# Kernel optimization log

Measured on AMD Instinct MI355X. Metric: run time of the kernel, lower is better.

Reference implementation:

```python
import jax, jax.numpy as jnp
import numpy as np

B, S, H, R = 2, 4096, 2048, 2048
NB, CW = 16, 4
BW = R // NB


def _block_diag_linear(x, w, b):
    # x: [B,S,R]; w: [NB,BW,BW]; b: [NB,BW]
    xb = x.reshape(x.shape[0], x.shape[1], NB, BW)
    out = jnp.einsum('bsni,nij->bsnj', xb, w) + b
    return out.reshape(x.shape)


def _causal_conv1d(x, conv_w, conv_b):
    # depthwise causal temporal conv: out[t] = sum_i w[i]*x[t-CW+1+i] + b
    xp = jnp.pad(x, ((0, 0), (CW - 1, 0), (0, 0)))
    out = conv_b
    for i in range(CW):
        out = out + conv_w[i] * xp[:, i:i + x.shape[1], :]
    return out


def _rg_lru_scan(x, x_gate_pre, a_gate_pre, a_param):
    gate_x = jax.nn.sigmoid(x_gate_pre)
    gate_a = jax.nn.sigmoid(a_gate_pre)
    log_a = -8.0 * gate_a * jax.nn.softplus(a_param)  # [B,S,R]
    a = jnp.exp(log_a)
    multiplier = jnp.sqrt(-jnp.expm1(2.0 * log_a))  # sqrt(1 - a^2)
    norm_x = x * gate_x * multiplier
    # h_t = a_t * h_{t-1} + norm_x_t via parallel associative scan over time
    def combine(c1, c2):
        a1, b1 = c1
        a2, b2 = c2
        return a1 * a2, a2 * b1 + b2
    _, h = jax.lax.associative_scan(combine, (a, norm_x), axis=1)
    return h


def setup_inputs() -> dict:
    key = jax.random.key(0)
    ks = jax.random.split(key, 9)
    x = jax.random.normal(ks[0], (B, S, H), dtype=jnp.float32)
    W_xy = jax.random.normal(ks[1], (2 * R, H), dtype=jnp.float32) / np.sqrt(H)
    ig_w = jax.random.normal(ks[2], (NB, BW, BW), dtype=jnp.float32) / np.sqrt(BW)
    ig_b = jnp.zeros((NB, BW), dtype=jnp.float32)
    ag_w = jax.random.normal(ks[3], (NB, BW, BW), dtype=jnp.float32) / np.sqrt(BW)
    ag_b = jnp.zeros((NB, BW), dtype=jnp.float32)
    # forget_init: a = a_real in [0.9, 0.999]; a_param = softplus^{-1}(-log(a_real))
    unif = jax.random.uniform(ks[4], (R,), dtype=jnp.float32)
    a_real = 0.5 * jnp.log(unif * (0.999 ** 2 - 0.9 ** 2) + 0.9 ** 2 + 1e-8)
    a_param = jnp.log(jnp.expm1(-a_real))
    conv_w = jax.random.normal(ks[5], (CW, R), dtype=jnp.float32) / np.sqrt(CW * R)
    conv_b = jnp.zeros((R,), dtype=jnp.float32)
    # resid_proj is zero-init in the module; use small random so output is non-trivial
    W_resid = 0.02 * jax.random.normal(ks[6], (H, R), dtype=jnp.float32)
    return {"x": x, "W_xy": W_xy, "ig_w": ig_w, "ig_b": ig_b,
            "ag_w": ag_w, "ag_b": ag_b, "a_param": a_param,
            "conv_w": conv_w, "conv_b": conv_b, "W_resid": W_resid}


def reference(x, W_xy, ig_w, ig_b, ag_w, ag_b, a_param, conv_w, conv_b, W_resid):
    xy = jnp.einsum('bsh,rh->bsr', x, W_xy)  # [B,S,2R]
    xr, y = jnp.split(xy, 2, axis=-1)
    xc = _causal_conv1d(xr, conv_w, conv_b)
    x_gate_pre = _block_diag_linear(xc, ig_w, ig_b)
    a_gate_pre = _block_diag_linear(xc, ag_w, ag_b)
    h = _rg_lru_scan(xc, x_gate_pre, a_gate_pre, a_param)
    out = jnp.einsum('bsr,hr->bsh', jax.nn.gelu(y, approximate=False) * h, W_resid)
    return out
```

## Files before the change

kernel.cpp:

```cpp
#include <hip/hip_runtime.h>
#include <hip/hip_bf16.h>

typedef __hip_bfloat16 bf16;
typedef __attribute__((ext_vector_type(8))) short s16x8;
typedef __attribute__((ext_vector_type(4))) float f32x4;

#define B_ 2
#define S_ 4096
#define H_ 2048
#define R_ 2048
#define M_ 8192
#define NB_ 16
#define BW_ 128
#define CHUNK 64
#define NCH 64

__device__ __forceinline__ short f2b_s(float f) {
    return (short)__builtin_bit_cast(unsigned short, __float2bfloat16(f));
}
__device__ __forceinline__ float b2f_s(short s) {
    unsigned int u = ((unsigned int)(unsigned short)s) << 16;
    return __builtin_bit_cast(float, u);
}
__device__ __forceinline__ float sigm_fast(float x) { return 1.f / (1.f + __expf(-x)); }

__device__ __forceinline__ void async_g2l(const void* g, void* l) {
    __builtin_amdgcn_global_load_lds((const __attribute__((address_space(1))) void*)g,
                                     (__attribute__((address_space(3))) void*)l, 16, 0, 0);
}

__global__ __launch_bounds__(256) void cast_all(const float* __restrict__ x,
                                                const float* __restrict__ wxy,
                                                const float* __restrict__ wres,
                                                bf16* __restrict__ xbf,
                                                bf16* __restrict__ wxyb,
                                                bf16* __restrict__ wresb) {
    int idx = blockIdx.x * 256 + threadIdx.x;
    const float* in; bf16* out; int off;
    if (idx < 2097152)      { in = x;    out = xbf;   off = idx; }
    else if (idx < 3145728) { in = wxy;  out = wxyb;  off = idx - 2097152; }
    else                    { in = wres; out = wresb; off = idx - 3145728; }
    size_t i8 = (size_t)off * 8;
    float4 v0 = *(const float4*)(in + i8);
    float4 v1 = *(const float4*)(in + i8 + 4);
    s16x8 o;
    o[0] = f2b_s(v0.x); o[1] = f2b_s(v0.y); o[2] = f2b_s(v0.z); o[3] = f2b_s(v0.w);
    o[4] = f2b_s(v1.x); o[5] = f2b_s(v1.y); o[6] = f2b_s(v1.z); o[7] = f2b_s(v1.w);
    *(s16x8*)(out + i8) = o;
}

__global__ __launch_bounds__(256) void wcast_T(const float* __restrict__ igw,
                                               const float* __restrict__ agw,
                                               bf16* __restrict__ wT) {
    __shared__ float tile[128 * 129];
    int blk = blockIdx.x;
    int p = blk >> 4, n = blk & 15;
    const float* w = (p ? agw : igw) + (size_t)n * 16384;
    int tid = threadIdx.x;
#pragma unroll
    for (int it = 0; it < 64; ++it) {
        int u = it * 256 + tid;
        tile[(u >> 7) * 129 + (u & 127)] = w[u];
    }
    __syncthreads();
    bf16* o = wT + (size_t)blk * 16384;
#pragma unroll
    for (int it = 0; it < 64; ++it) {
        int u = it * 256 + tid;
        o[u] = __float2bfloat16(tile[(u & 127) * 129 + (u >> 7)]);
    }
}

__global__ __launch_bounds__(256) void sp8_kernel(const float* __restrict__ apar,
                                                  float* __restrict__ sp8) {
    int r = blockIdx.x * 256 + threadIdx.x;
    float ap = apar[r];
    sp8[r] = 8.f * (ap > 20.f ? ap : log1pf(expf(ap)));
}

__device__ __forceinline__ void store_c(float* p, float v) { *p = v; }
__device__ __forceinline__ void store_c(bf16* p, float v) { *p = __float2bfloat16(v); }

template <typename OutT>
__global__ __launch_bounds__(256, 4) void gemm_bt(const bf16* __restrict__ A,
                                                  const bf16* __restrict__ Bm,
                                                  OutT* __restrict__ C,
                                                  int K, int lda, int ldb, int ldc) {
    __shared__ __align__(16) short As[128 * 64];
    __shared__ __align__(16) short Bs[128 * 64];
    const int tid = threadIdx.x;
    const int lane = tid & 63, wave = tid >> 6;
    const int waveM = wave >> 1, waveN = wave & 1;
    const int mBase = blockIdx.y * 128, nBase = blockIdx.x * 128;
    const int fm = lane & 15, q = lane >> 4;

    f32x4 acc[4][4];
#pragma unroll
    for (int i = 0; i < 4; ++i)
#pragma unroll
        for (int j = 0; j < 4; ++j) acc[i][j] = (f32x4){0.f, 0.f, 0.f, 0.f};

    for (int k0 = 0; k0 < K; k0 += 64) {
        __syncthreads();
#pragma unroll
        for (int it = 0; it < 4; ++it) {
            int off = it * 4096 + tid * 16;
            int r = off >> 7;
            int g = ((off & 127) >> 4) ^ (r & 7);
            async_g2l(A + (size_t)(mBase + r) * lda + k0 + g * 8, (char*)As + off);
            async_g2l(Bm + (size_t)(nBase + r) * ldb + k0 + g * 8, (char*)Bs + off);
        }
        __syncthreads();
#pragma unroll
        for (int s = 0; s < 2; ++s) {
            s16x8 af[4], bfr[4];
#pragma unroll
            for (int i = 0; i < 4; ++i) {
                int row = waveM * 64 + i * 16 + fm;
                af[i] = *(const s16x8*)((char*)As + row * 128 + ((((s << 2) + q) ^ (row & 7)) << 4));
                int col = waveN * 64 + i * 16 + fm;
                bfr[i] = *(const s16x8*)((char*)Bs + col * 128 + ((((s << 2) + q) ^ (col & 7)) << 4));
            }
#pragma unroll
            for (int i = 0; i < 4; ++i)
#pragma unroll
                for (int j = 0; j < 4; ++j)
                    acc[i][j] = __builtin_amdgcn_mfma_f32_16x16x32_bf16(af[i], bfr[j], acc[i][j], 0, 0, 0);
        }
    }
#pragma unroll
    for (int i = 0; i < 4; ++i) {
        int rowg = mBase + waveM * 64 + i * 16 + q * 4;
#pragma unroll
        for (int j = 0; j < 4; ++j) {
            int colg = nBase + waveN * 64 + j * 16 + fm;
#pragma unroll
            for (int rr = 0; rr < 4; ++rr)
                store_c(C + (size_t)(rowg + rr) * ldc + colg, acc[i][j][rr]);
        }
    }
}

__global__ __launch_bounds__(256) void gate_kernel(const bf16* __restrict__ xy,
                                                   const float* __restrict__ cw,
                                                   const float* __restrict__ cb,
                                                   const bf16* __restrict__ wT,
                                                   const float* __restrict__ igb,
                                                   const float* __restrict__ agb,
                                                   const float* __restrict__ sp8,
                                                   bf16* __restrict__ hloc_out,
                                                   bf16* __restrict__ cum_out,
                                                   float* __restrict__ Ach,
                                                   float* __restrict__ Hla) {
    __shared__ __align__(16) short As[64 * 128];
    __shared__ __align__(16) char  Wmem[128 * 256];
    short* Xs   = (short*)Wmem;
    short* Ws   = (short*)Wmem;
    float* a_sh = (float*)Wmem;
    const int n = blockIdx.x;
    const int mBase = blockIdx.y * 64;
    const int tid = threadIdx.x;
    const int lane = tid & 63, wave = tid >> 6;
    const int fm = lane & 15, q = lane >> 4;
    const int t0 = mBase & (S_ - 1);

#pragma unroll
    for (int it = 0; it < 5; ++it) {
        int u = it * 256 + tid;
        if (u < 67 * 16) {
            int rr = u >> 4, gg = u & 15;
            s16x8 v = (s16x8){0, 0, 0, 0, 0, 0, 0, 0};
            if (t0 != 0 || rr >= 3) {
                int m = mBase + rr - 3;
                v = *(const s16x8*)(xy + (size_t)m * 4096 + n * BW_ + gg * 8);
            }
            *(s16x8*)((char*)Xs + u * 16) = v;
        }
    }
    __syncthreads();

    {
        int col = tid & 127, rh = tid >> 7;
        int rbase = n * BW_ + col;
        float w0c = cw[rbase], w1c = cw[R_ + rbase], w2c = cw[2 * R_ + rbase],
              w3c = cw[3 * R_ + rbase];
        float bc = cb[rbase];
        int r0 = rh * 32;
        float xm3 = b2f_s(Xs[(r0 + 0) * 128 + col]);
        float xm2 = b2f_s(Xs[(r0 + 1) * 128 + col]);
        float xm1 = b2f_s(Xs[(r0 + 2) * 128 + col]);
#pragma unroll
        for (int rw = 0; rw < 32; ++rw) {
            int row = r0 + rw;
            float x0 = b2f_s(Xs[(row + 3) * 128 + col]);
            float v = bc + w0c * xm3 + w1c * xm2 + w2c * xm1 + w3c * x0;
            xm3 = xm2; xm2 = xm1; xm1 = x0;
            *(short*)((char*)As + row * 256 + ((((col >> 3)) ^ (row & 15)) << 4) +
                      (col & 7) * 2) = f2b_s(v);
        }
    }
    __syncthreads();

    const bf16* w0 = wT + (size_t)n * 16384;
#pragma unroll
    for (int it = 0; it < 8; ++it) {
        int off = it * 4096 + tid * 16;
        int j = off >> 8;
        int g = ((off & 255) >> 4) ^ (j & 15);
        async_g2l(w0 + j * 128 + g * 8, (char*)Ws + off);
    }
    __syncthreads();

    f32x4 accI[8], accA[8];
#pragma unroll
    for (int jj = 0; jj < 8; ++jj) {
        accI[jj] = (f32x4){0.f, 0.f, 0.f, 0.f};
        accA[jj] = (f32x4){0.f, 0.f, 0.f, 0.f};
    }

    const int row = wave * 16 + fm;
#pragma unroll
    for (int s = 0; s < 4; ++s) {
        s16x8 af = *(const s16x8*)((char*)As + row * 256 + ((((s << 2) + q) ^ (row & 15)) << 4));
#pragma unroll
        for (int jj = 0; jj < 8; ++jj) {
            int wrow = jj * 16 + fm;
            s16x8 bw = *(const s16x8*)((char*)Ws + wrow * 256 + ((((s << 2) + q) ^ (wrow & 15)) << 4));
            accI[jj] = __builtin_amdgcn_mfma_f32_16x16x32_bf16(af, bw, accI[jj], 0, 0, 0);
        }
    }
    __syncthreads();
    const bf16* w1 = wT + (size_t)(NB_ + n) * 16384;
#pragma unroll
    for (int it = 0; it < 8; ++it) {
        int off = it * 4096 + tid * 16;
        int j = off >> 8;
        int g = ((off & 255) >> 4) ^ (j & 15);
        async_g2l(w1 + j * 128 + g * 8, (char*)Ws + off);
    }
    __syncthreads();
#pragma unroll
    for (int s = 0; s < 4; ++s) {
        s16x8 af = *(const s16x8*)((char*)As + row * 256 + ((((s << 2) + q) ^ (row & 15)) << 4));
#pragma unroll
        for (int jj = 0; jj < 8; ++jj) {
            int wrow = jj * 16 + fm;
            s16x8 bw = *(const s16x8*)((char*)Ws + wrow * 256 + ((((s << 2) + q) ^ (wrow & 15)) << 4));
            accA[jj] = __builtin_amdgcn_mfma_f32_16x16x32_bf16(af, bw, accA[jj], 0, 0, 0);
        }
    }
    __syncthreads();

#pragma unroll
    for (int jj = 0; jj < 8; ++jj) {
        int col = jj * 16 + fm;
        int r = n * BW_ + col;
        float bi = igb[r], ba = agb[r];
        float s8 = sp8[r];
#pragma unroll
        for (int rr = 0; rr < 4; ++rr) {
            int rowl = wave * 16 + q * 4 + rr;
            short* slot = (short*)((char*)As + rowl * 256 +
                          ((((col >> 3)) ^ (rowl & 15)) << 4) + (col & 7) * 2);
            float xcv = b2f_s(*slot);
            float xg = accI[jj][rr] + bi;
            float ag = accA[jj][rr] + ba;
            float la = -s8 * sigm_fast(ag);
            float av = __expf(la);
            float t2 = 2.f * la;
            float nem = (t2 > -0.125f)
                ? -t2 * (1.f + t2 * (0.5f + t2 * (0.16666667f + t2 * 0.04166667f)))
                : 1.f - av * av;
            float nxv = xcv * sigm_fast(xg) * sqrtf(nem);
            short nxs = f2b_s(nxv);
            a_sh[rowl * 128 + col] = av;
            *slot = nxs;
        }
    }
    __syncthreads();

    if (tid < 128) {
        int col = tid;
        float h = 0.f, cum = 1.f;
        size_t o = (size_t)mBase * R_ + n * BW_ + col;
#pragma unroll 4
        for (int t = 0; t < CHUNK; ++t) {
            float a = a_sh[t * 128 + col];
            float nxv = b2f_s(*(const short*)((char*)As + t * 256 +
                              ((((col >> 3)) ^ (t & 15)) << 4) + (col & 7) * 2));
            h = fmaf(a, h, nxv);
            cum *= a;
            hloc_out[o] = __float2bfloat16(h);
            cum_out[o]  = __float2bfloat16(cum);
            o += R_;
        }
        int b = mBase >> 12, c = (mBase & (S_ - 1)) >> 6;
        int so = ((b * NCH + c) << 11) + n * BW_ + col;
        Ach[so] = cum;
        Hla[so] = h;
    }
}

__global__ __launch_bounds__(256) void scan_carry(const float* __restrict__ Ach,
                                                  const float* __restrict__ Hla,
                                                  float* __restrict__ carry) {
    int idx = blockIdx.x * 256 + threadIdx.x;
    int r = idx & (R_ - 1), b = idx >> 11;
    float cy = 0.f;
#pragma unroll 4
    for (int c = 0; c < NCH; ++c) {
        int o = (b * NCH + c) * R_ + r;
        carry[o] = cy;
        cy = fmaf(Ach[o], cy, Hla[o]);
    }
}

__global__ __launch_bounds__(256) void scan_passB(const bf16* __restrict__ hloc,
                                                  const bf16* __restrict__ cum,
                                                  const float* __restrict__ carry,
                                                  const bf16* __restrict__ xy,
                                                  bf16* __restrict__ g_out) {
    int idx = blockIdx.x * 256 + threadIdx.x;
    int m = idx >> 8;
    int r = (idx & 255) << 3;
    int b = m >> 12, c = (m & 4095) >> 6;
    int so = ((b * NCH + c) << 11) + r;
    size_t o = (size_t)m * R_ + r;
    s16x8 hv = *(const s16x8*)(hloc + o);
    s16x8 cv = *(const s16x8*)(cum + o);
    float4 cy0 = *(const float4*)(carry + so);
    float4 cy1 = *(const float4*)(carry + so + 4);
    s16x8 yv = *(const s16x8*)(xy + (size_t)m * 4096 + 2048 + r);
    float cya0 = cy0.x, cya1 = cy0.y, cya2 = cy0.z, cya3 = cy0.w;
    float cya4 = cy1.x, cya5 = cy1.y, cya6 = cy1.z, cya7 = cy1.w;
    s16x8 g;
#pragma unroll 8
    for (int i = 0; i < 8; ++i) {
        float cy = (i == 0) ? cya0 : (i == 1) ? cya1 : (i == 2) ? cya2 : (i == 3) ? cya3
                 : (i == 4) ? cya4 : (i == 5) ? cya5 : (i == 6) ? cya6 : cya7;
        float h = fmaf(b2f_s(cv[i]), cy, b2f_s(hv[i]));
        float y = b2f_s(yv[i]);
        float gg = 0.5f * y * (1.f + erff(y * 0.70710678f));
        g[i] = f2b_s(gg * h);
    }
    *(s16x8*)(g_out + o) = g;
}

extern "C" void kernel_launch(void* const* d_in, const int* in_sizes, int n_in,
                              void* d_out, int out_size, void* d_ws, size_t ws_size,
                              hipStream_t stream) {
    const float* x    = (const float*)d_in[0];
    const float* Wxy  = (const float*)d_in[1];
    const float* igw  = (const float*)d_in[2];
    const float* igb  = (const float*)d_in[3];
    const float* agw  = (const float*)d_in[4];
    const float* agb  = (const float*)d_in[5];
    const float* apar = (const float*)d_in[6];
    const float* cw   = (const float*)d_in[7];
    const float* cb   = (const float*)d_in[8];
    const float* Wres = (const float*)d_in[9];
    float* out = (float*)d_out;

    char* ws = (char*)d_ws;
    const size_t MiB = (size_t)1 << 20;
    bf16*  xbf   = (bf16*)(ws);
    bf16*  hloc  = (bf16*)(ws);
    bf16*  wxyb  = (bf16*)(ws + 32 * MiB);
    bf16*  wT    = (bf16*)(ws + 32 * MiB);
    float* sp8   = (float*)(ws + 33 * MiB + 65536);
    bf16*  xy    = (bf16*)(ws + 48 * MiB);
    bf16*  wresb = (bf16*)(ws + 112 * MiB);
    bf16*  g     = (bf16*)(ws + 120 * MiB);
    bf16*  cum   = (bf16*)(ws + 152 * MiB);
    float* Ach   = (float*)(ws + 184 * MiB);
    float* Hla   = (float*)(ws + 185 * MiB);
    float* cyb   = (float*)(ws + 186 * MiB);

    cast_all<<<14336, 256, 0, stream>>>(x, Wxy, Wres, xbf, wxyb, wresb);

    gemm_bt<bf16><<<dim3(32, 64), 256, 0, stream>>>(xbf, wxyb, xy, 2048, 2048, 2048, 4096);

    wcast_T<<<32, 256, 0, stream>>>(igw, agw, wT);
    sp8_kernel<<<8, 256, 0, stream>>>(apar, sp8);

    gate_kernel<<<dim3(NB_, 128), 256, 0, stream>>>(xy, cw, cb, wT, igb, agb, sp8,
                                                    hloc, cum, Ach, Hla);

    scan_carry<<<16, 256, 0, stream>>>(Ach, Hla, cyb);
    scan_passB<<<8192, 256, 0, stream>>>(hloc, cum, cyb, xy, g);

    gemm_bt<float><<<dim3(16, 64), 256, 0, stream>>>(g, wresb, out, 2048, 2048, 2048, 2048);
}
```

Before: 463.5 us.

## Replace 128x128 GEMM with 256x256 double-buffered, phase-pipelined 8-wave kernel

```diff
diff --git a/kernel.cpp b/kernel.cpp
--- a/kernel.cpp
+++ b/kernel.cpp
@@ -81,59 +81,116 @@
 __device__ __forceinline__ void store_c(float* p, float v) { *p = v; }
 __device__ __forceinline__ void store_c(bf16* p, float v) { *p = __float2bfloat16(v); }
 
+#define MFMA16(Q)                                                                     \
+    _Pragma("unroll") for (int j = 0; j < 4; ++j) {                                   \
+        acc[2*(Q)][j]   = __builtin_amdgcn_mfma_f32_16x16x32_bf16(af[0][0], bfr[j][0], acc[2*(Q)][j], 0, 0, 0);   \
+        acc[2*(Q)][j]   = __builtin_amdgcn_mfma_f32_16x16x32_bf16(af[0][1], bfr[j][1], acc[2*(Q)][j], 0, 0, 0);   \
+        acc[2*(Q)+1][j] = __builtin_amdgcn_mfma_f32_16x16x32_bf16(af[1][0], bfr[j][0], acc[2*(Q)+1][j], 0, 0, 0); \
+        acc[2*(Q)+1][j] = __builtin_amdgcn_mfma_f32_16x16x32_bf16(af[1][1], bfr[j][1], acc[2*(Q)+1][j], 0, 0, 0); \
+    }
+
+#define PHASE(BASEP, Q, LOADB, STMTS, VMSTMT)                                         \
+    rdA2(BASEP, Q, af);                                                               \
+    if (LOADB) rdB8(BASEP, bfr);                                                      \
+    STMTS;                                                                            \
+    if (LOADB) asm volatile("s_waitcnt lgkmcnt(8)" ::: "memory");                     \
+    __builtin_amdgcn_s_barrier();                                                     \
+    asm volatile("s_waitcnt lgkmcnt(0)" ::: "memory");                                \
+    __builtin_amdgcn_sched_barrier(0);                                                \
+    __builtin_amdgcn_s_setprio(1);                                                    \
+    MFMA16(Q);                                                                        \
+    __builtin_amdgcn_s_setprio(0);                                                    \
+    VMSTMT;                                                                           \
+    __builtin_amdgcn_s_barrier();                                                     \
+    __builtin_amdgcn_sched_barrier(0);
+
 template <typename OutT>
-__global__ __launch_bounds__(256, 4) void gemm_bt(const bf16* __restrict__ A,
+__global__ __launch_bounds__(512, 2) void gemm256(const bf16* __restrict__ A,
                                                   const bf16* __restrict__ Bm,
                                                   OutT* __restrict__ C,
                                                   int K, int lda, int ldb, int ldc) {
-    __shared__ __align__(16) short As[128 * 64];
-    __shared__ __align__(16) short Bs[128 * 64];
+    extern __shared__ __align__(16) char lds[];
     const int tid = threadIdx.x;
     const int lane = tid & 63, wave = tid >> 6;
-    const int waveM = wave >> 1, waveN = wave & 1;
-    const int mBase = blockIdx.y * 128, nBase = blockIdx.x * 128;
+    const int wm = wave >> 2, wn = wave & 3;
     const int fm = lane & 15, q = lane >> 4;
-
-    f32x4 acc[4][4];
-#pragma unroll
-    for (int i = 0; i < 4; ++i)
+    const int mBase = blockIdx.y * 256, nBase = blockIdx.x * 256;
+    const int NT = K >> 6, LT = (NT >> 1) - 1;
+
+    auto stage_half = [&](int tile, int hh) {
+        if (tile >= NT) return;
+        const bf16* src = (hh < 2) ? Bm : A;
+        const int ld = (hh < 2) ? ldb : lda;
+        const int rowBase = ((hh < 2) ? nBase : mBase) + ((hh & 1) << 7);
+        char* dst = lds + ((tile & 1) << 16) + ((hh < 2) ? 32768 : 0) + ((hh & 1) << 14);
+#pragma unroll
+        for (int rnd = 0; rnd < 2; ++rnd) {
+            int off = rnd * 8192 + tid * 16;
+            int r = off >> 7;
+            int g = ((off >> 4) & 7) ^ (r & 7);
+            async_g2l(src + (size_t)(rowBase + r) * ld + tile * 64 + g * 8, dst + off);
+        }
+    };
+    auto rdA2 = [&](const char* base, int qp, s16x8 (&dst)[2][2]) {
+#pragma unroll
+        for (int i2 = 0; i2 < 2; ++i2) {
+            int r7 = (qp * 2 + i2) * 16 + fm;
+            const char* p = base + (wm << 14) + r7 * 128;
+#pragma unroll
+            for (int kk = 0; kk < 2; ++kk)
+                dst[i2][kk] = *(const s16x8*)(p + ((((kk << 2) + q) ^ (r7 & 7)) << 4));
+        }
+    };
+    auto rdB8 = [&](const char* base, s16x8 (&dst)[4][2]) {
+#pragma unroll
+        for (int j = 0; j < 4; ++j) {
+            int col = wn * 64 + j * 16 + fm;
+            const char* p = base + 32768 + ((col >> 7) << 14) + (col & 127) * 128;
+#pragma unroll
+            for (int kk = 0; kk < 2; ++kk)
+                dst[j][kk] = *(const s16x8*)(p + ((((kk << 2) + q) ^ (col & 7)) << 4));
+        }
+    };
+
+    s16x8 af[2][2], bfr[4][2];
+    f32x4 acc[8][4];
+#pragma unroll
+    for (int i = 0; i < 8; ++i)
 #pragma unroll
         for (int j = 0; j < 4; ++j) acc[i][j] = (f32x4){0.f, 0.f, 0.f, 0.f};
 
-    for (int k0 = 0; k0 < K; k0 += 64) {
-        __syncthreads();
-#pragma unroll
-        for (int it = 0; it < 4; ++it) {
-            int off = it * 4096 + tid * 16;
-            int r = off >> 7;
-            int g = ((off & 127) >> 4) ^ (r & 7);
-            async_g2l(A + (size_t)(mBase + r) * lda + k0 + g * 8, (char*)As + off);
-            async_g2l(Bm + (size_t)(nBase + r) * ldb + k0 + g * 8, (char*)Bs + off);
-        }
-        __syncthreads();
-#pragma unroll
-        for (int s = 0; s < 2; ++s) {
-            s16x8 af[4], bfr[4];
-#pragma unroll
-            for (int i = 0; i < 4; ++i) {
-                int row = waveM * 64 + i * 16 + fm;
-                af[i] = *(const s16x8*)((char*)As + row * 128 + ((((s << 2) + q) ^ (row & 7)) << 4));
-                int col = waveN * 64 + i * 16 + fm;
-                bfr[i] = *(const s16x8*)((char*)Bs + col * 128 + ((((s << 2) + q) ^ (col & 7)) << 4));
-            }
-#pragma unroll
-            for (int i = 0; i < 4; ++i)
-#pragma unroll
-                for (int j = 0; j < 4; ++j)
-                    acc[i][j] = __builtin_amdgcn_mfma_f32_16x16x32_bf16(af[i], bfr[j], acc[i][j], 0, 0, 0);
-        }
-    }
-#pragma unroll
-    for (int i = 0; i < 4; ++i) {
-        int rowg = mBase + waveM * 64 + i * 16 + q * 4;
+    stage_half(0, 0); stage_half(0, 1); stage_half(0, 2); stage_half(0, 3);
+    stage_half(1, 0); stage_half(1, 1);
+    asm volatile("s_waitcnt vmcnt(4)" ::: "memory");
+    __builtin_amdgcn_s_barrier();
+    __builtin_amdgcn_sched_barrier(0);
+
+    for (int t = 0; t <= LT; ++t) {
+        const int Ta = 2 * t, Tb = Ta + 1;
+        const char* b0 = lds;
+        const char* b1 = lds + 65536;
+
+        PHASE(b0, 0, 1, { stage_half(Tb, 2); }, {})
+        PHASE(b0, 1, 0, { stage_half(Tb, 3); stage_half(Ta + 2, 0); }, {})
+        PHASE(b0, 2, 0, { stage_half(Ta + 2, 1); }, {})
+        PHASE(b0, 3, 0, {},
+              { if (t < LT) asm volatile("s_waitcnt vmcnt(4)" ::: "memory");
+                else        asm volatile("s_waitcnt vmcnt(0)" ::: "memory"); })
+
+        PHASE(b1, 0, 1, { stage_half(Ta + 2, 2); }, {})
+        PHASE(b1, 1, 0, { stage_half(Ta + 2, 3); stage_half(Tb + 2, 0); }, {})
+        PHASE(b1, 2, 0, { stage_half(Tb + 2, 1); }, {})
+        PHASE(b1, 3, 0, {},
+              { if (t < LT) asm volatile("s_waitcnt vmcnt(4)" ::: "memory");
+                else        asm volatile("s_waitcnt vmcnt(0)" ::: "memory"); })
+    }
+
+#pragma unroll
+    for (int i = 0; i < 8; ++i) {
+        int rowg = mBase + wm * 128 + i * 16 + q * 4;
 #pragma unroll
         for (int j = 0; j < 4; ++j) {
-            int colg = nBase + waveN * 64 + j * 16 + fm;
+            int colg = nBase + wn * 64 + j * 16 + fm;
 #pragma unroll
             for (int rr = 0; rr < 4; ++rr)
                 store_c(C + (size_t)(rowg + rr) * ldc + colg, acc[i][j][rr]);
@@ -378,7 +435,7 @@
 
     cast_all<<<14336, 256, 0, stream>>>(x, Wxy, Wres, xbf, wxyb, wresb);
 
-    gemm_bt<bf16><<<dim3(32, 64), 256, 0, stream>>>(xbf, wxyb, xy, 2048, 2048, 2048, 4096);
+    gemm256<bf16><<<dim3(16, 32), 512, 131072, stream>>>(xbf, wxyb, xy, 2048, 2048, 2048, 4096);
 
     wcast_T<<<32, 256, 0, stream>>>(igw, agw, wT);
     sp8_kernel<<<8, 256, 0, stream>>>(apar, sp8);
@@ -389,5 +446,5 @@
     scan_carry<<<16, 256, 0, stream>>>(Ach, Hla, cyb);
     scan_passB<<<8192, 256, 0, stream>>>(hloc, cum, cyb, xy, g);
 
-    gemm_bt<float><<<dim3(16, 64), 256, 0, stream>>>(g, wresb, out, 2048, 2048, 2048, 2048);
-}
+    gemm256<float><<<dim3(8, 32), 512, 131072, stream>>>(g, wresb, out, 2048, 2048, 2048, 2048);
+}
```

Measured after the change: 455.9 us. About the same (-1.6%).
